# Kernel tuning notes

Measured on AMD Instinct MI355X. Metric: run time of the kernel, lower is better.

The kernel has to match this reference:

```python
import jax, jax.numpy as jnp
import numpy as np

HID = 1024
HEADS = 16
HEAD_DIM = HID // HEADS


def setup_inputs() -> dict:
    key = jax.random.key(0)
    ks = jax.random.split(key, 11)
    s = 1.0 / np.sqrt(HID)
    return {
        "query": jax.random.normal(ks[0], (4, 2048, HID), jnp.float32),
        "key": jax.random.normal(ks[1], (4, 2048, HID), jnp.float32),
        "value": jax.random.normal(ks[2], (4, 2048, HID), jnp.float32),
        "wq": jax.random.normal(ks[3], (HID, HID), jnp.float32) * s,
        "bq": jnp.zeros((HID,), jnp.float32),
        "wk": jax.random.normal(ks[4], (HID, HID), jnp.float32) * s,
        "bk": jnp.zeros((HID,), jnp.float32),
        "wv": jax.random.normal(ks[5], (HID, HID), jnp.float32) * s,
        "bv": jnp.zeros((HID,), jnp.float32),
        "wo": jax.random.normal(ks[6], (HID, HID), jnp.float32) * s,
        "bo": jnp.zeros((HID,), jnp.float32),
    }


def reference(query, key, value, wq, bq, wk, bk, wv, bv, wo, bo):
    b, s, _ = query.shape
    scale = jnp.sqrt(jnp.asarray(HEAD_DIM, query.dtype))
    # linear projections; weights stored as [in, out]
    Q = (query @ wq + bq).reshape(b, s, HEADS, HEAD_DIM).transpose(0, 2, 1, 3)
    K = (key @ wk + bk).reshape(b, s, HEADS, HEAD_DIM).transpose(0, 2, 1, 3)
    V = (value @ wv + bv).reshape(b, s, HEADS, HEAD_DIM).transpose(0, 2, 1, 3)
    energy = jnp.einsum('bhqd,bhkd->bhqk', Q, K) / scale  # [B,H,S,S]
    attention = jax.nn.softmax(energy, axis=-1)  # dropout p=0 -> identity
    x = jnp.einsum('bhqk,bhkd->bhqd', attention, V)
    x = x.transpose(0, 2, 1, 3).reshape(b, s, HID)
    return x @ wo + bo
```

## Files before the change

### kernel.cpp

```cpp
#include <hip/hip_runtime.h>
#include <hip/hip_bf16.h>

#define B_   4
#define S_   2048
#define HID_ 1024
#define H_   16
#define D_   64
#define M_   (B_ * S_)

typedef __attribute__((ext_vector_type(8)))  short bf16x8;
typedef __attribute__((ext_vector_type(4)))  float f32x4;
typedef __attribute__((ext_vector_type(16))) float f32x16;

#define GAS __attribute__((address_space(1)))
#define LAS __attribute__((address_space(3)))

__device__ __forceinline__ unsigned short f2bf(float f) {
    union { float f; unsigned int u; } x; x.f = f;
    unsigned int u = x.u;
    return (unsigned short)((u + 0x7fffu + ((u >> 16) & 1u)) >> 16);
}

__global__ __launch_bounds__(256)
void cast3(const float* __restrict__ q, const float* __restrict__ k, const float* __restrict__ v,
           unsigned short* __restrict__ oq, unsigned short* __restrict__ ok,
           unsigned short* __restrict__ ov) {
    const int sel = blockIdx.x >> 12;
    const int i = (blockIdx.x & 4095) * 256 + threadIdx.x;
    const float* in = (sel == 0) ? q : (sel == 1) ? k : v;
    unsigned short* out = (sel == 0) ? oq : (sel == 1) ? ok : ov;
    const f32x4 a = ((const f32x4*)in)[i * 2];
    const f32x4 b = ((const f32x4*)in)[i * 2 + 1];
    bf16x8 w;
#pragma unroll
    for (int j = 0; j < 4; j++) { w[j] = (short)f2bf(a[j]); w[4 + j] = (short)f2bf(b[j]); }
    ((bf16x8*)out)[i] = w;
}

__global__ void transpose_cast(const float* __restrict__ w0, const float* __restrict__ w1,
                               const float* __restrict__ w2, const float* __restrict__ w3,
                               unsigned short* __restrict__ o0, unsigned short* __restrict__ o1,
                               unsigned short* __restrict__ o2, unsigned short* __restrict__ o3) {
    __shared__ float t[32][33];
    const float* w = (blockIdx.z == 0) ? w0 : (blockIdx.z == 1) ? w1 : (blockIdx.z == 2) ? w2 : w3;
    unsigned short* o = (blockIdx.z == 0) ? o0 : (blockIdx.z == 1) ? o1 : (blockIdx.z == 2) ? o2 : o3;
    const int tx = threadIdx.x, ty = threadIdx.y;
    const int bx = blockIdx.x * 32, by = blockIdx.y * 32;
#pragma unroll
    for (int i = 0; i < 4; i++)
        t[ty + i * 8][tx] = w[(size_t)(by + ty + i * 8) * HID_ + bx + tx];
    __syncthreads();
#pragma unroll
    for (int i = 0; i < 4; i++)
        o[(size_t)(bx + ty + i * 8) * HID_ + by + tx] = f2bf(t[tx][ty + i * 8]);
}

__global__ __launch_bounds__(256, 3)
void gemm_qkv(const unsigned short* __restrict__ aq, const unsigned short* __restrict__ ak,
              const unsigned short* __restrict__ av, const unsigned short* __restrict__ wqkvT,
              const float* __restrict__ bq, const float* __restrict__ bk,
              const float* __restrict__ bv, unsigned short* __restrict__ Qp,
              unsigned short* __restrict__ Kp, unsigned short* __restrict__ Vt, float cvt) {
    constexpr int BK = 32;
    __shared__ unsigned short smem[8704];
    unsigned short* As = smem;
    unsigned short* Bs = smem + 4096;

    const int tid  = threadIdx.x;
    const int lane = tid & 63;
    const int wave = tid >> 6;
    const int quad = lane >> 4;
    const int col  = lane & 15;
    const int wr   = (wave & 1) * 64;
    const int wc   = (wave >> 1) * 64;
    const int m0   = blockIdx.x * 128;
    const int third = blockIdx.y >> 3;
    const int n0l   = (blockIdx.y & 7) * 128;
    const bool vmode = (third == 2);

    const unsigned short* act = (third == 0) ? aq : (third == 1) ? ak : av;
    const float* bias = (third == 0) ? bq : (third == 1) ? bk : bv;
    unsigned short* outp = (third == 0) ? Qp : (third == 1) ? Kp : Vt;
    const float oscale = (third == 0) ? cvt : 1.f;

    const int grow = wave * 16 + (lane >> 2);
    const int gcol = (lane & 3) * 8;
    const unsigned short* wgp = wqkvT + (size_t)(third * HID_ + n0l + grow) * HID_ + gcol;
    const unsigned short* agp = act + (size_t)(m0 + grow) * HID_ + gcol;
    const unsigned short* rgp = vmode ? agp : wgp;
    const unsigned short* cgp = vmode ? wgp : agp;
    unsigned short* asb = &As[wave * 512];
    unsigned short* bsb = &Bs[wave * 512];

    f32x4 zero; zero[0] = 0.f; zero[1] = 0.f; zero[2] = 0.f; zero[3] = 0.f;
    f32x4 acc[4][4];
#pragma unroll
    for (int ri = 0; ri < 4; ri++)
#pragma unroll
        for (int ci = 0; ci < 4; ci++) acc[ri][ci] = zero;

    for (int kt = 0; kt < HID_; kt += BK) {
        __builtin_amdgcn_global_load_lds((const GAS unsigned int*)(rgp + kt),
                                         (LAS unsigned int*)asb, 16, 0, 0);
        __builtin_amdgcn_global_load_lds((const GAS unsigned int*)(rgp + kt + (size_t)64 * HID_),
                                         (LAS unsigned int*)(asb + 2048), 16, 0, 0);
        __builtin_amdgcn_global_load_lds((const GAS unsigned int*)(cgp + kt),
                                         (LAS unsigned int*)bsb, 16, 0, 0);
        __builtin_amdgcn_global_load_lds((const GAS unsigned int*)(cgp + kt + (size_t)64 * HID_),
                                         (LAS unsigned int*)(bsb + 2048), 16, 0, 0);
        __syncthreads();

        bf16x8 af[4], cf[4];
#pragma unroll
        for (int i = 0; i < 4; i++) af[i] = *(const bf16x8*)&As[(wr + i * 16 + col) * BK + quad * 8];
#pragma unroll
        for (int i = 0; i < 4; i++) cf[i] = *(const bf16x8*)&Bs[(wc + i * 16 + col) * BK + quad * 8];
#pragma unroll
        for (int ri = 0; ri < 4; ri++)
#pragma unroll
            for (int ci = 0; ci < 4; ci++)
                acc[ri][ci] = __builtin_amdgcn_mfma_f32_16x16x32_bf16(af[ri], cf[ci], acc[ri][ci], 0, 0, 0);
        __syncthreads();
    }

    unsigned short* RB = smem;
#pragma unroll
    for (int ph = 0; ph < 2; ph++) {
        if ((wave >> 1) == ph) {
#pragma unroll
            for (int ri = 0; ri < 4; ri++) {
                f32x4 bv4;
                if (!vmode) bv4 = *(const f32x4*)&bias[n0l + wr + ri * 16 + quad * 4];
#pragma unroll
                for (int ci = 0; ci < 4; ci++) {
                    float b0, b1, b2, b3;
                    if (!vmode) { b0 = bv4[0]; b1 = bv4[1]; b2 = bv4[2]; b3 = bv4[3]; }
                    else { b0 = b1 = b2 = b3 = bias[n0l + wc + ci * 16 + col]; }
                    const unsigned int u0 = f2bf((acc[ri][ci][0] + b0) * oscale);
                    const unsigned int u1 = f2bf((acc[ri][ci][1] + b1) * oscale);
                    const unsigned int u2 = f2bf((acc[ri][ci][2] + b2) * oscale);
                    const unsigned int u3 = f2bf((acc[ri][ci][3] + b3) * oscale);
                    uint2 w; w.x = u0 | (u1 << 16); w.y = u2 | (u3 << 16);
                    *(uint2*)&RB[(ci * 16 + col) * 136 + wr + ri * 16 + quad * 4] = w;
                }
            }
        }
        __syncthreads();
#pragma unroll
        for (int it = 0; it < 4; it++) {
            const int c   = it * 256 + tid;
            const int row = c >> 4, ch = c & 15;
            const bf16x8 v = *(const bf16x8*)&RB[row * 136 + ch * 8];
            if (!vmode) {
                const int n = n0l + ch * 8;
                const int h = n >> 6, d = n & 63;
                const int m = m0 + ph * 64 + row;
                *(bf16x8*)&outp[(((size_t)(m >> 11) * H_ + h) * S_ + (m & 2047)) * D_ + d] = v;
            } else {
                const int m = m0 + ch * 8;
                const int n = n0l + ph * 64 + row;
                const int h = n >> 6, d = n & 63;
                *(bf16x8*)&outp[(((size_t)(m >> 11) * H_ + h) * D_ + d) * S_ + (m & 2047)] = v;
            }
        }
        __syncthreads();
    }
}

__global__ __launch_bounds__(256, 3)
void gemm_o(const unsigned short* __restrict__ A, const unsigned short* __restrict__ Bt,
            const float* __restrict__ bias, float* __restrict__ outp) {
    constexpr int BK = 32;
    __shared__ float smemf[64 * 132];
    unsigned short* As = (unsigned short*)smemf;
    unsigned short* Bs = As + 4096;

    const int tid  = threadIdx.x;
    const int lane = tid & 63;
    const int wave = tid >> 6;
    const int quad = lane >> 4;
    const int col  = lane & 15;
    const int wn   = (wave >> 1) * 64;
    const int wm   = (wave & 1) * 64;
    const int m0   = blockIdx.x * 128;
    const int n0l  = blockIdx.y * 128;

    const int grow = wave * 16 + (lane >> 2);
    const int gcol = (lane & 3) * 8;
    const unsigned short* agp = A + (size_t)(m0 + grow) * HID_ + gcol;
    const unsigned short* wgp = Bt + (size_t)(n0l + grow) * HID_ + gcol;
    unsigned short* asb = &As[wave * 512];
    unsigned short* bsb = &Bs[wave * 512];

    f32x4 zero; zero[0] = 0.f; zero[1] = 0.f; zero[2] = 0.f; zero[3] = 0.f;
    f32x4 acc[4][4];
#pragma unroll
    for (int ri = 0; ri < 4; ri++)
#pragma unroll
        for (int ci = 0; ci < 4; ci++) acc[ri][ci] = zero;

    for (int kt = 0; kt < HID_; kt += BK) {
        __builtin_amdgcn_global_load_lds((const GAS unsigned int*)(wgp + kt),
                                         (LAS unsigned int*)asb, 16, 0, 0);
        __builtin_amdgcn_global_load_lds((const GAS unsigned int*)(wgp + kt + (size_t)64 * HID_),
                                         (LAS unsigned int*)(asb + 2048), 16, 0, 0);
        __builtin_amdgcn_global_load_lds((const GAS unsigned int*)(agp + kt),
                                         (LAS unsigned int*)bsb, 16, 0, 0);
        __builtin_amdgcn_global_load_lds((const GAS unsigned int*)(agp + kt + (size_t)64 * HID_),
                                         (LAS unsigned int*)(bsb + 2048), 16, 0, 0);
        __syncthreads();

        bf16x8 wf[4], af[4];
#pragma unroll
        for (int i = 0; i < 4; i++) wf[i] = *(const bf16x8*)&As[(wn + i * 16 + col) * BK + quad * 8];
#pragma unroll
        for (int i = 0; i < 4; i++) af[i] = *(const bf16x8*)&Bs[(wm + i * 16 + col) * BK + quad * 8];
#pragma unroll
        for (int ri = 0; ri < 4; ri++)
#pragma unroll
            for (int ci = 0; ci < 4; ci++)
                acc[ri][ci] = __builtin_amdgcn_mfma_f32_16x16x32_bf16(wf[ri], af[ci], acc[ri][ci], 0, 0, 0);
        __syncthreads();
    }

#pragma unroll
    for (int ph = 0; ph < 2; ph++) {
        if ((wave & 1) == ph) {
#pragma unroll
            for (int ri = 0; ri < 4; ri++) {
                const f32x4 bv4 = *(const f32x4*)&bias[n0l + wn + ri * 16 + quad * 4];
#pragma unroll
                for (int ci = 0; ci < 4; ci++) {
                    f32x4 v;
#pragma unroll
                    for (int i = 0; i < 4; i++) v[i] = acc[ri][ci][i] + bv4[i];
                    *(f32x4*)&smemf[(ci * 16 + col) * 132 + wn + ri * 16 + quad * 4] = v;
                }
            }
        }
        __syncthreads();
#pragma unroll
        for (int it = 0; it < 8; it++) {
            const int c   = it * 256 + tid;
            const int row = c >> 5, ch = c & 31;
            const f32x4 v = *(const f32x4*)&smemf[row * 132 + ch * 4];
            *(f32x4*)&outp[(size_t)(m0 + ph * 64 + row) * HID_ + n0l + ch * 4] = v;
        }
        __syncthreads();
    }
}

__global__ __launch_bounds__(256)
void attn_k(const unsigned short* __restrict__ Qp, const unsigned short* __restrict__ Kp,
            const unsigned short* __restrict__ Vt, unsigned short* __restrict__ Xc) {
    constexpr int LT = 72;
    __shared__ unsigned short Ks[64 * LT];
    __shared__ unsigned short Vs[64 * LT];
    __shared__ unsigned short Pb[4 * 32 * LT];

    const int tid  = threadIdx.x;
    const int lane = tid & 63;
    const int wave = tid >> 6;
    const int l31  = lane & 31;
    const int hw   = lane >> 5;
    const int bh   = blockIdx.y;
    const int q0   = blockIdx.x * 128 + wave * 32;

    const unsigned short* Qb = Qp + (size_t)bh * S_ * D_;
    const unsigned short* Kb = Kp + (size_t)bh * S_ * D_;
    const unsigned short* Vb = Vt + (size_t)bh * D_ * S_;

    bf16x8 qf[4];
#pragma unroll
    for (int ks = 0; ks < 4; ks++)
        qf[ks] = *(const bf16x8*)&Qb[(q0 + l31) * D_ + ks * 16 + hw * 8];

    f32x16 o[2];
#pragma unroll
    for (int t = 0; t < 2; t++)
#pragma unroll
        for (int i = 0; i < 16; i++) o[t][i] = 0.f;
    float lpart = 0.f;
    unsigned short* Pw = &Pb[wave * 32 * LT];

    for (int c0 = 0; c0 < S_; c0 += 64) {
#pragma unroll
        for (int it = 0; it < 2; it++) {
            const int c = it * 256 + tid;
            const int row = c >> 3, seg = (c & 7) * 8;
            *(bf16x8*)&Ks[row * LT + seg] = *(const bf16x8*)&Kb[(size_t)(c0 + row) * D_ + seg];
            *(bf16x8*)&Vs[row * LT + seg] = *(const bf16x8*)&Vb[(size_t)row * S_ + c0 + seg];
        }
        __syncthreads();

#pragma unroll
        for (int g = 0; g < 2; g++) {
            f32x16 e;
#pragma unroll
            for (int i = 0; i < 16; i++) e[i] = 0.f;
#pragma unroll
            for (int ks = 0; ks < 4; ks++) {
                const bf16x8 a = *(const bf16x8*)&Ks[(g * 32 + l31) * LT + ks * 16 + hw * 8];
                e = __builtin_amdgcn_mfma_f32_32x32x16_bf16(a, qf[ks], e, 0, 0, 0);
            }
#pragma unroll
            for (int grp = 0; grp < 4; grp++) {
                float p0 = __builtin_amdgcn_exp2f(e[grp * 4 + 0]);
                float p1 = __builtin_amdgcn_exp2f(e[grp * 4 + 1]);
                float p2 = __builtin_amdgcn_exp2f(e[grp * 4 + 2]);
                float p3 = __builtin_amdgcn_exp2f(e[grp * 4 + 3]);
                lpart += (p0 + p1) + (p2 + p3);
                const unsigned int u0 = __builtin_bit_cast(unsigned int, p0) + 0x8000u;
                const unsigned int u1 = __builtin_bit_cast(unsigned int, p1) + 0x8000u;
                const unsigned int u2 = __builtin_bit_cast(unsigned int, p2) + 0x8000u;
                const unsigned int u3 = __builtin_bit_cast(unsigned int, p3) + 0x8000u;
                uint2 w;
                w.x = __builtin_amdgcn_perm(u1, u0, 0x07060302u);
                w.y = __builtin_amdgcn_perm(u3, u2, 0x07060302u);
                *(uint2*)&Pw[l31 * LT + g * 32 + grp * 8 + hw * 4] = w;
            }
        }

#pragma unroll
        for (int ks = 0; ks < 4; ks++) {
            const bf16x8 pf = *(const bf16x8*)&Pw[l31 * LT + ks * 16 + hw * 8];
#pragma unroll
            for (int t = 0; t < 2; t++) {
                const bf16x8 vf = *(const bf16x8*)&Vs[(t * 32 + l31) * LT + ks * 16 + hw * 8];
                o[t] = __builtin_amdgcn_mfma_f32_32x32x16_bf16(vf, pf, o[t], 0, 0, 0);
            }
        }
        __syncthreads();
    }

    float l = lpart;
    l += __shfl_xor(l, 32);
    const float inv = 1.f / l;

    const int b = bh >> 4, h = bh & 15;
    const int s = q0 + l31;
    unsigned short* xp = &Xc[((size_t)(b * S_ + s)) * HID_ + h * D_];
#pragma unroll
    for (int t = 0; t < 2; t++)
#pragma unroll
        for (int grp = 0; grp < 4; grp++) {
            const unsigned int u0 = f2bf(o[t][grp * 4 + 0] * inv);
            const unsigned int u1 = f2bf(o[t][grp * 4 + 1] * inv);
            const unsigned int u2 = f2bf(o[t][grp * 4 + 2] * inv);
            const unsigned int u3 = f2bf(o[t][grp * 4 + 3] * inv);
            uint2 w; w.x = u0 | (u1 << 16); w.y = u2 | (u3 << 16);
            *(uint2*)&xp[t * 32 + grp * 8 + hw * 4] = w;
        }
}

extern "C" void kernel_launch(void* const* d_in, const int* in_sizes, int n_in,
                              void* d_out, int out_size, void* d_ws, size_t ws_size,
                              hipStream_t stream) {
    (void)in_sizes; (void)n_in; (void)out_size; (void)ws_size;
    const float* query = (const float*)d_in[0];
    const float* key   = (const float*)d_in[1];
    const float* value = (const float*)d_in[2];
    const float* wq    = (const float*)d_in[3];
    const float* bq    = (const float*)d_in[4];
    const float* wk    = (const float*)d_in[5];
    const float* bk    = (const float*)d_in[6];
    const float* wv    = (const float*)d_in[7];
    const float* bv    = (const float*)d_in[8];
    const float* wo    = (const float*)d_in[9];
    const float* bo    = (const float*)d_in[10];
    float* out = (float*)d_out;

    unsigned short* ws  = (unsigned short*)d_ws;
    const size_t WSZ = (size_t)HID_ * HID_;
    const size_t TSZ = (size_t)M_ * HID_;
    unsigned short* wqkvT = ws;
    unsigned short* woT = ws + 3 * WSZ;
    unsigned short* Qp  = woT + WSZ;
    unsigned short* Kp  = Qp + TSZ;
    unsigned short* Vt  = Kp + TSZ;
    unsigned short* Xc  = Vt + TSZ;
    unsigned short* Xb  = Xc + TSZ;

    const float cvt = 0.125f * 1.44269504f;

    transpose_cast<<<dim3(32, 32, 4), dim3(32, 8), 0, stream>>>(
        wq, wk, wv, wo, wqkvT, wqkvT + WSZ, wqkvT + 2 * WSZ, woT);

    cast3<<<3 * 4096, 256, 0, stream>>>(query, key, value, Xc, Xb, Xb + TSZ);

    gemm_qkv<<<dim3(M_ / 128, 24), 256, 0, stream>>>(
        Xc, Xb, Xb + TSZ, wqkvT, bq, bk, bv, Qp, Kp, Vt, cvt);

    attn_k<<<dim3(S_ / 128, B_ * H_), 256, 0, stream>>>(Qp, Kp, Vt, Xc);

    gemm_o<<<dim3(M_ / 128, 8), 256, 0, stream>>>(Xc, woT, bo, out);
}
```

Baseline: 360.1 us.

## Double-buffer K/V tiles with register prefetch and keep P in registers

The attention kernel now double-buffers the K and V LDS tiles, prefetching the next tile into registers and storing it into the alternate buffer, so only one barrier per iteration remains and global load latency overlaps compute. The P tile no longer round-trips through shared memory. It is converted with v_cvt_pk_bf16_f32 and rearranged across half-waves with v_permlane32_swap so it can feed the PV MFMA directly. Launch bounds now request occupancy 4, which raises register pressure from the prefetch registers and risks spills.

Result: faster. 350.7 us (-2.6%).

```diff
diff --git a/kernel.cpp b/kernel.cpp
--- a/kernel.cpp
+++ b/kernel.cpp
@@ -250,13 +250,13 @@
     }
 }
 
-__global__ __launch_bounds__(256)
+__global__ __launch_bounds__(256, 4)
 void attn_k(const unsigned short* __restrict__ Qp, const unsigned short* __restrict__ Kp,
             const unsigned short* __restrict__ Vt, unsigned short* __restrict__ Xc) {
     constexpr int LT = 72;
-    __shared__ unsigned short Ks[64 * LT];
-    __shared__ unsigned short Vs[64 * LT];
-    __shared__ unsigned short Pb[4 * 32 * LT];
+    constexpr int NT = S_ / 64;
+    __shared__ unsigned short Ks[2][64 * LT];
+    __shared__ unsigned short Vs[2][64 * LT];
 
     const int tid  = threadIdx.x;
     const int lane = tid & 63;
@@ -281,18 +281,33 @@
 #pragma unroll
         for (int i = 0; i < 16; i++) o[t][i] = 0.f;
     float lpart = 0.f;
-    unsigned short* Pw = &Pb[wave * 32 * LT];
-
-    for (int c0 = 0; c0 < S_; c0 += 64) {
-#pragma unroll
-        for (int it = 0; it < 2; it++) {
-            const int c = it * 256 + tid;
-            const int row = c >> 3, seg = (c & 7) * 8;
-            *(bf16x8*)&Ks[row * LT + seg] = *(const bf16x8*)&Kb[(size_t)(c0 + row) * D_ + seg];
-            *(bf16x8*)&Vs[row * LT + seg] = *(const bf16x8*)&Vb[(size_t)row * S_ + c0 + seg];
-        }
-        __syncthreads();
-
+
+    const int srow = tid >> 3;
+    const int seg  = (tid & 7) * 8;
+    bf16x8 kr[2], vr[2];
+
+#pragma unroll
+    for (int it = 0; it < 2; it++) {
+        const int row = it * 32 + srow;
+        kr[it] = *(const bf16x8*)&Kb[(size_t)row * D_ + seg];
+        vr[it] = *(const bf16x8*)&Vb[(size_t)row * S_ + seg];
+    }
+#pragma unroll
+    for (int it = 0; it < 2; it++) {
+        const int row = it * 32 + srow;
+        *(bf16x8*)&Ks[0][row * LT + seg] = kr[it];
+        *(bf16x8*)&Vs[0][row * LT + seg] = vr[it];
+    }
+#pragma unroll
+    for (int it = 0; it < 2; it++) {
+        const int row = it * 32 + srow;
+        kr[it] = *(const bf16x8*)&Kb[(size_t)(64 + row) * D_ + seg];
+        vr[it] = *(const bf16x8*)&Vb[(size_t)row * S_ + 64 + seg];
+    }
+    __syncthreads();
+
+    for (int t = 0; t < NT; ++t) {
+        const int cur = t & 1;
 #pragma unroll
         for (int g = 0; g < 2; g++) {
             f32x16 e;
@@ -300,34 +315,52 @@
             for (int i = 0; i < 16; i++) e[i] = 0.f;
 #pragma unroll
             for (int ks = 0; ks < 4; ks++) {
-                const bf16x8 a = *(const bf16x8*)&Ks[(g * 32 + l31) * LT + ks * 16 + hw * 8];
+                const bf16x8 a = *(const bf16x8*)&Ks[cur][(g * 32 + l31) * LT + ks * 16 + hw * 8];
                 e = __builtin_amdgcn_mfma_f32_32x32x16_bf16(a, qf[ks], e, 0, 0, 0);
             }
+            unsigned int ulo[4], uhi[4];
 #pragma unroll
             for (int grp = 0; grp < 4; grp++) {
-                float p0 = __builtin_amdgcn_exp2f(e[grp * 4 + 0]);
-                float p1 = __builtin_amdgcn_exp2f(e[grp * 4 + 1]);
-                float p2 = __builtin_amdgcn_exp2f(e[grp * 4 + 2]);
-                float p3 = __builtin_amdgcn_exp2f(e[grp * 4 + 3]);
+                const float p0 = __builtin_amdgcn_exp2f(e[grp * 4 + 0]);
+                const float p1 = __builtin_amdgcn_exp2f(e[grp * 4 + 1]);
+                const float p2 = __builtin_amdgcn_exp2f(e[grp * 4 + 2]);
+                const float p3 = __builtin_amdgcn_exp2f(e[grp * 4 + 3]);
                 lpart += (p0 + p1) + (p2 + p3);
-                const unsigned int u0 = __builtin_bit_cast(unsigned int, p0) + 0x8000u;
-                const unsigned int u1 = __builtin_bit_cast(unsigned int, p1) + 0x8000u;
-                const unsigned int u2 = __builtin_bit_cast(unsigned int, p2) + 0x8000u;
-                const unsigned int u3 = __builtin_bit_cast(unsigned int, p3) + 0x8000u;
-                uint2 w;
-                w.x = __builtin_amdgcn_perm(u1, u0, 0x07060302u);
-                w.y = __builtin_amdgcn_perm(u3, u2, 0x07060302u);
-                *(uint2*)&Pw[l31 * LT + g * 32 + grp * 8 + hw * 4] = w;
-            }
-        }
-
-#pragma unroll
-        for (int ks = 0; ks < 4; ks++) {
-            const bf16x8 pf = *(const bf16x8*)&Pw[l31 * LT + ks * 16 + hw * 8];
-#pragma unroll
-            for (int t = 0; t < 2; t++) {
-                const bf16x8 vf = *(const bf16x8*)&Vs[(t * 32 + l31) * LT + ks * 16 + hw * 8];
-                o[t] = __builtin_amdgcn_mfma_f32_32x32x16_bf16(vf, pf, o[t], 0, 0, 0);
+                asm("v_cvt_pk_bf16_f32 %0, %1, %2" : "=v"(ulo[grp]) : "v"(p0), "v"(p1));
+                asm("v_cvt_pk_bf16_f32 %0, %1, %2" : "=v"(uhi[grp]) : "v"(p2), "v"(p3));
+            }
+#pragma unroll
+            for (int sub = 0; sub < 2; sub++) {
+                unsigned int w0 = ulo[2 * sub], w2 = ulo[2 * sub + 1];
+                unsigned int w1 = uhi[2 * sub], w3 = uhi[2 * sub + 1];
+                asm("v_permlane32_swap_b32 %0, %1" : "+v"(w0), "+v"(w2));
+                asm("v_permlane32_swap_b32 %0, %1" : "+v"(w1), "+v"(w3));
+                union { unsigned int u[4]; bf16x8 v; } pf;
+                pf.u[0] = w0; pf.u[1] = w1; pf.u[2] = w2; pf.u[3] = w3;
+                const int ks = g * 2 + sub;
+#pragma unroll
+                for (int tt = 0; tt < 2; tt++) {
+                    const bf16x8 vf = *(const bf16x8*)&Vs[cur][(tt * 32 + l31) * LT + ks * 16 + hw * 8];
+                    o[tt] = __builtin_amdgcn_mfma_f32_32x32x16_bf16(vf, pf.v, o[tt], 0, 0, 0);
+                }
+            }
+        }
+
+        if (t + 1 < NT) {
+#pragma unroll
+            for (int it = 0; it < 2; it++) {
+                const int row = it * 32 + srow;
+                *(bf16x8*)&Ks[cur ^ 1][row * LT + seg] = kr[it];
+                *(bf16x8*)&Vs[cur ^ 1][row * LT + seg] = vr[it];
+            }
+            if (t + 2 < NT) {
+                const int c0 = (t + 2) * 64;
+#pragma unroll
+                for (int it = 0; it < 2; it++) {
+                    const int row = it * 32 + srow;
+                    kr[it] = *(const bf16x8*)&Kb[(size_t)(c0 + row) * D_ + seg];
+                    vr[it] = *(const bf16x8*)&Vb[(size_t)row * S_ + c0 + seg];
+                }
             }
         }
         __syncthreads();
```
